# Performance work log

Hardware: AMD Instinct MI355X
Metric: run time of the kernel (lower is better)

Reference implementation:

```python
import jax, jax.numpy as jnp
import numpy as np

B, H, D, RD = 32, 16, 256, 64          # batch, heads, head_dim, rotary_dim
NE, NI = 4096, 16384                   # n_embd, n_inner
SLOTS, KVL = 32768, 1024               # paged cache slots, per-batch kv length
EPS = 1e-5


def setup_inputs() -> dict:
    key = jax.random.key(0)
    ks = jax.random.split(key, 12)
    s = 0.02
    return {
        "hidden_states": jax.random.normal(ks[0], (B, 1, NE), jnp.float32),
        "key_cache": jax.random.normal(ks[1], (SLOTS, H, D), jnp.float32),
        "value_cache": jax.random.normal(ks[2], (SLOTS, H, D), jnp.float32),
        "ln_w": jnp.ones((NE,), jnp.float32),
        "ln_b": jnp.zeros((NE,), jnp.float32),
        "wq": jax.random.normal(ks[3], (NE, NE), jnp.float32) * s,
        "wk": jax.random.normal(ks[4], (NE, NE), jnp.float32) * s,
        "wv": jax.random.normal(ks[5], (NE, NE), jnp.float32) * s,
        "wo": jax.random.normal(ks[6], (NE, NE), jnp.float32) * s,
        "fc_in_w": jax.random.normal(ks[7], (NE, NI), jnp.float32) * s,
        "fc_in_b": jnp.zeros((NI,), jnp.float32),
        "fc_out_w": jax.random.normal(ks[8], (NI, NE), jnp.float32) * s,
        "fc_out_b": jnp.zeros((NE,), jnp.float32),
        "attention_mask": jnp.zeros((B, 1, 1, KVL), jnp.float32),
        "new_key_location": jnp.arange(B, dtype=jnp.int32),
        "new_value_location": jnp.arange(B, dtype=jnp.int32),
        "past_valid_key_decode_indices": jax.random.randint(ks[9], (B, KVL), 0, SLOTS, jnp.int32),
        "past_valid_value_decode_indices": jax.random.randint(ks[10], (B, KVL), 0, SLOTS, jnp.int32),
        "position_ids": jax.random.randint(ks[11], (B, 1), 0, KVL, jnp.int32),
    }


def _rope(x, position_ids):
    # GPT-J rotate-every-two rotary on first RD dims. x: [B, S, H, D]
    half = RD // 2
    inv_freq = 1.0 / (10000.0 ** (jnp.arange(0, RD, 2, dtype=jnp.float32) / RD))  # [half]
    ang = position_ids.astype(jnp.float32)[..., None] * inv_freq  # [B, S, half]
    sin = jnp.sin(ang)[:, :, None, :]  # [B, S, 1, half]
    cos = jnp.cos(ang)[:, :, None, :]
    xr, xp = x[..., :RD], x[..., RD:]
    x1, x2 = xr[..., 0::2], xr[..., 1::2]
    o1 = x1 * cos - x2 * sin
    o2 = x2 * cos + x1 * sin
    rot = jnp.stack([o1, o2], axis=-1).reshape(xr.shape)
    return jnp.concatenate([rot, xp], axis=-1)


def reference(hidden_states, key_cache, value_cache, ln_w, ln_b, wq, wk, wv, wo,
              fc_in_w, fc_in_b, fc_out_w, fc_out_b, attention_mask,
              new_key_location, new_value_location,
              past_valid_key_decode_indices, past_valid_value_decode_indices,
              position_ids):
    residual = hidden_states[:, -1:, :]                       # [B, 1, NE]
    mu = jnp.mean(hidden_states, axis=-1, keepdims=True)
    var = jnp.mean(jnp.square(hidden_states - mu), axis=-1, keepdims=True)
    h = (hidden_states - mu) * jax.lax.rsqrt(var + EPS) * ln_w + ln_b

    q = (h @ wq).reshape(B, 1, H, D)
    k = (h @ wk).reshape(B, 1, H, D)
    v = (h @ wv).reshape(B, 1, H, D)
    q = _rope(q, position_ids)
    k = _rope(k, position_ids)

    # paged KV update: scatter new token, gather valid slots per batch
    kc = key_cache.at[new_key_location].set(k[:, 0])          # [SLOTS, H, D]
    vc = value_cache.at[new_value_location].set(v[:, 0])
    K = kc[past_valid_key_decode_indices]                     # [B, KVL, H, D]
    V = vc[past_valid_value_decode_indices]                   # [B, KVL, H, D]

    scale = jnp.asarray(np.sqrt(D), jnp.float32)
    scores = jnp.einsum("bqhd,blhd->bhql", q, K) / scale + attention_mask
    p = jax.nn.softmax(scores, axis=-1)                       # [B, H, 1, KVL]
    ctx = jnp.einsum("bhql,blhd->bqhd", p, V).reshape(B, 1, NE)
    attn_out = ctx @ wo

    m = jax.nn.gelu(h[:, -1:, :] @ fc_in_w + fc_in_b, approximate=True)
    mlp_out = m @ fc_out_w + fc_out_b

    return attn_out + mlp_out + residual
```

## Files before the change

### kernel.cpp

```cpp
#include <hip/hip_runtime.h>
#include <math.h>

#define BB 32
#define HH 16
#define DD 256
#define RDIM 64
#define NEMB 4096
#define NINT 16384
#define NSLOTS 32768
#define KVLEN 1024
#define LNEPS 1e-5f
#define NCH 16
#define CH 64

__global__ __launch_bounds__(256) void ln_kernel(const float* __restrict__ x,
    const float* __restrict__ lw, const float* __restrict__ lb,
    float* __restrict__ hT)
{
    int b = blockIdx.x;
    int t = threadIdx.x;
    const float* row = x + (size_t)b * NEMB;
    float4 v[4];
    float sum = 0.f, sq = 0.f;
#pragma unroll
    for (int j = 0; j < 4; ++j) {
        v[j] = *(const float4*)(row + t * 4 + j * 1024);
        sum += v[j].x + v[j].y + v[j].z + v[j].w;
        sq += v[j].x * v[j].x + v[j].y * v[j].y + v[j].z * v[j].z + v[j].w * v[j].w;
    }
    __shared__ float s1[4], s2[4];
#pragma unroll
    for (int o = 32; o > 0; o >>= 1) {
        sum += __shfl_xor(sum, o, 64);
        sq += __shfl_xor(sq, o, 64);
    }
    int wave = t >> 6, lane = t & 63;
    if (lane == 0) { s1[wave] = sum; s2[wave] = sq; }
    __syncthreads();
    sum = s1[0] + s1[1] + s1[2] + s1[3];
    sq = s2[0] + s2[1] + s2[2] + s2[3];
    float mu = sum / NEMB;
    float var = sq / NEMB - mu * mu;
    float rstd = rsqrtf(var + LNEPS);
#pragma unroll
    for (int j = 0; j < 4; ++j) {
        int n = t * 4 + j * 1024;
        float4 wv = *(const float4*)(lw + n);
        float4 bv = *(const float4*)(lb + n);
        hT[(size_t)(n + 0) * BB + b] = (v[j].x - mu) * rstd * wv.x + bv.x;
        hT[(size_t)(n + 1) * BB + b] = (v[j].y - mu) * rstd * wv.y + bv.y;
        hT[(size_t)(n + 2) * BB + b] = (v[j].z - mu) * rstd * wv.z + bv.z;
        hT[(size_t)(n + 3) * BB + b] = (v[j].w - mu) * rstd * wv.w + bv.w;
    }
}

__device__ __forceinline__ void gemm_body(const float* __restrict__ AT,
    const float* __restrict__ W, float* __restrict__ P,
    int N, int kChunk, int x, int s)
{
    int n = (x * 256 + threadIdx.x) * 2;
    size_t k0 = (size_t)s * kChunk;
    float2 acc[32];
#pragma unroll
    for (int mi = 0; mi < 32; ++mi) acc[mi] = make_float2(0.f, 0.f);
    const float* w = W + k0 * N + n;
    const float* a = AT + k0 * 32;
#pragma unroll 4
    for (int kk = 0; kk < kChunk; ++kk) {
        float2 wv = *(const float2*)w;
#pragma unroll
        for (int mi = 0; mi < 32; ++mi) {
            float am = a[mi];
            acc[mi].x = fmaf(am, wv.x, acc[mi].x);
            acc[mi].y = fmaf(am, wv.y, acc[mi].y);
        }
        w += N;
        a += 32;
    }
    float* p = P + ((size_t)s * 32) * N + n;
#pragma unroll
    for (int mi = 0; mi < 32; ++mi)
        *(float2*)(p + (size_t)mi * N) = acc[mi];
}

__global__ __launch_bounds__(256) void phase2_kernel(const float* __restrict__ hT,
    const float* __restrict__ wq, const float* __restrict__ wk, const float* __restrict__ wv,
    float* __restrict__ Pq, const float* __restrict__ fciw, float* __restrict__ P1)
{
    int id = blockIdx.x;
    if (id < 768) {
        int w = id >> 8;
        const float* W = (w == 0) ? wq : (w == 1) ? wk : wv;
        float* Pz = Pq + (size_t)w * ((size_t)32 * 32 * NEMB);
        gemm_body(hT, W, Pz, NEMB, 128, id & 7, (id >> 3) & 31);
    } else {
        id -= 768;
        gemm_body(hT, fciw, P1, NINT, 256, id & 31, id >> 5);
    }
}

__device__ inline float gelu_tanh(float x)
{
    float x3 = x * x * x;
    return 0.5f * x * (1.f + tanhf(0.7978845608028654f * (x + 0.044715f * x3)));
}

__global__ __launch_bounds__(256) void phase3_kernel(const float* __restrict__ Pq,
    float* __restrict__ q, float* __restrict__ k, float* __restrict__ v,
    const int* __restrict__ pos,
    const float* __restrict__ P1, const float* __restrict__ fcib, float* __restrict__ mT)
{
    int id = blockIdx.x, t = threadIdx.x;
    if (id < 768) {
        int w = id >> 8;
        int m = (id >> 3) & 31;
        int n0 = ((id & 7) * 256 + t) * 2;
        const float* p = Pq + (size_t)w * ((size_t)32 * 32 * NEMB) + (size_t)m * NEMB + n0;
        float sx = 0.f, sy = 0.f;
#pragma unroll 4
        for (int i = 0; i < 32; ++i) {
            float2 u = *(const float2*)p;
            sx += u.x; sy += u.y;
            p += (size_t)32 * NEMB;
        }
        int d = n0 & (DD - 1);
        if (w < 2 && d < RDIM) {
            int i = d >> 1;
            float fr = exp2f((float)i * (-13.287712379549449f / 32.f));
            float ang = (float)pos[m] * fr;
            float sn, cs;
            sincosf(ang, &sn, &cs);
            float x1 = sx, x2 = sy;
            sx = x1 * cs - x2 * sn;
            sy = x2 * cs + x1 * sn;
        }
        float* o = (w == 0) ? q : (w == 1) ? k : v;
        *(float2*)(o + (size_t)m * NEMB + n0) = make_float2(sx, sy);
    } else {
        int j = id - 768;
        int m = j >> 6;
        int n = (j & 63) * 256 + t;
        const float* p = P1 + (size_t)m * NINT + n;
        float s = 0.f;
#pragma unroll 4
        for (int i = 0; i < 16; ++i) { s += *p; p += (size_t)32 * NINT; }
        mT[(size_t)n * 32 + m] = gelu_tanh(s + fcib[n]);
    }
}

__global__ __launch_bounds__(256) void phase4_kernel(const float* __restrict__ q,
    const float* __restrict__ knew, const float* __restrict__ vnew,
    const float* __restrict__ kcache, const float* __restrict__ vcache,
    const int* __restrict__ kidx, const int* __restrict__ vidx,
    const int* __restrict__ nkl, const int* __restrict__ nvl,
    const float* __restrict__ mask,
    float* __restrict__ pm, float* __restrict__ pl, float* __restrict__ pctx,
    const float* __restrict__ mT, const float* __restrict__ fcow, float* __restrict__ P2)
{
    int id = blockIdx.x;
    if (id >= 8192) {
        int j = id - 8192;
        gemm_body(mT, fcow, P2, NEMB, 256, j & 7, j >> 3);
        return;
    }
    int bh = id >> 4, c = id & 15;
    int b = bh >> 4, h = bh & 15;
    int t = threadIdx.x;
    __shared__ float qs[DD];
    __shared__ float sc[CH];
    __shared__ const float* kp[CH];
    __shared__ const float* vp[CH];
    __shared__ float cx[4][DD];

    qs[t] = q[(size_t)b * NEMB + (size_t)h * DD + t];
    if (t < CH) {
        int l = c * CH + t;
        int ks = kidx[b * KVLEN + l];
        int vs = vidx[b * KVLEN + l];
        const float* kbase = kcache + (size_t)ks * NEMB;
        const float* vbase = vcache + (size_t)vs * NEMB;
#pragma unroll
        for (int j = 0; j < BB; ++j) {
            if (nkl[j] == ks) kbase = knew + (size_t)j * NEMB;
            if (nvl[j] == vs) vbase = vnew + (size_t)j * NEMB;
        }
        kp[t] = kbase + (size_t)h * DD;
        vp[t] = vbase + (size_t)h * DD;
    }
    __syncthreads();

    int wave = t >> 6, lane = t & 63;
    int g = lane >> 4, u = lane & 15;

    float4 qf[4];
#pragma unroll
    for (int j = 0; j < 4; ++j) qf[j] = *(const float4*)(qs + u * 4 + j * 64);

#pragma unroll
    for (int it = 0; it < 4; ++it) {
        int l = it * 16 + wave * 4 + g;
        const float* kr = kp[l];
        float d = 0.f;
#pragma unroll
        for (int j = 0; j < 4; ++j) {
            float4 kf = *(const float4*)(kr + u * 4 + j * 64);
            d = fmaf(kf.x, qf[j].x, fmaf(kf.y, qf[j].y, fmaf(kf.z, qf[j].z, fmaf(kf.w, qf[j].w, d))));
        }
        d += __shfl_xor(d, 8, 64);
        d += __shfl_xor(d, 4, 64);
        d += __shfl_xor(d, 2, 64);
        d += __shfl_xor(d, 1, 64);
        if (u == 0) sc[l] = d * 0.0625f + mask[b * KVLEN + c * CH + l];
    }
    __syncthreads();

    float sv = sc[lane];
    float mx = sv;
#pragma unroll
    for (int o = 32; o > 0; o >>= 1) mx = fmaxf(mx, __shfl_xor(mx, o, 64));
    float e = expf(sv - mx);
    float sm = e;
#pragma unroll
    for (int o = 32; o > 0; o >>= 1) sm += __shfl_xor(sm, o, 64);

    float4 a4 = make_float4(0.f, 0.f, 0.f, 0.f);
#pragma unroll 8
    for (int l = wave; l < CH; l += 4) {
        float4 vf = *(const float4*)(vp[l] + lane * 4);
        float pw = __shfl(e, l, 64);
        a4.x = fmaf(pw, vf.x, a4.x);
        a4.y = fmaf(pw, vf.y, a4.y);
        a4.z = fmaf(pw, vf.z, a4.z);
        a4.w = fmaf(pw, vf.w, a4.w);
    }
    *(float4*)(&cx[wave][lane * 4]) = a4;
    __syncthreads();

    int pi = bh * NCH + c;
    pctx[(size_t)pi * DD + t] = cx[0][t] + cx[1][t] + cx[2][t] + cx[3][t];
    if (t == 0) { pm[pi] = mx; pl[pi] = sm; }
}

__global__ __launch_bounds__(256) void attn_comb_kernel(const float* __restrict__ pm,
    const float* __restrict__ pl, const float* __restrict__ pctx,
    float* __restrict__ ctxT)
{
    int bh = blockIdx.x;
    int b = bh >> 4, h = bh & 15;
    int t = threadIdx.x;
    float M = -INFINITY;
#pragma unroll
    for (int c = 0; c < NCH; ++c) M = fmaxf(M, pm[bh * NCH + c]);
    float L = 0.f, acc = 0.f;
#pragma unroll
    for (int c = 0; c < NCH; ++c) {
        float wv = expf(pm[bh * NCH + c] - M);
        L += pl[bh * NCH + c] * wv;
        acc += pctx[((size_t)bh * NCH + c) * DD + t] * wv;
    }
    ctxT[((size_t)h * DD + t) * BB + b] = acc / L;
}

__global__ __launch_bounds__(256) void phase6_kernel(const float* __restrict__ ctxT,
    const float* __restrict__ wo, float* __restrict__ P0,
    const float* __restrict__ P2, const float* __restrict__ fcob,
    const float* __restrict__ resid, float* __restrict__ mlp_tmp)
{
    int id = blockIdx.x, t = threadIdx.x;
    if (id < 512) {
        gemm_body(ctxT, wo, P0, NEMB, 64, id & 7, id >> 3);
    } else {
        int j = id - 512;
        int m = j >> 4;
        int n = (j & 15) * 256 + t;
        const float* p = P2 + (size_t)m * NEMB + n;
        float s = 0.f;
#pragma unroll 4
        for (int i = 0; i < 64; ++i) { s += *p; p += (size_t)32 * NEMB; }
        mlp_tmp[(size_t)m * NEMB + n] = s + fcob[n] + resid[(size_t)m * NEMB + n];
    }
}

__global__ __launch_bounds__(256) void phase7_kernel(const float* __restrict__ P0,
    const float* __restrict__ mlp_tmp, float* __restrict__ out)
{
    int n = blockIdx.x * 256 + threadIdx.x;
    int m = blockIdx.y;
    const float* p = P0 + (size_t)m * NEMB + n;
    float s = 0.f;
#pragma unroll 4
    for (int i = 0; i < 64; ++i) { s += *p; p += (size_t)32 * NEMB; }
    out[(size_t)m * NEMB + n] = s + mlp_tmp[(size_t)m * NEMB + n];
}

extern "C" void kernel_launch(void* const* d_in, const int* in_sizes, int n_in,
                              void* d_out, int out_size, void* d_ws, size_t ws_size,
                              hipStream_t stream)
{
    (void)in_sizes; (void)n_in; (void)out_size; (void)ws_size;
    const float* hs      = (const float*)d_in[0];
    const float* kcache  = (const float*)d_in[1];
    const float* vcache  = (const float*)d_in[2];
    const float* ln_w    = (const float*)d_in[3];
    const float* ln_b    = (const float*)d_in[4];
    const float* wq      = (const float*)d_in[5];
    const float* wk      = (const float*)d_in[6];
    const float* wv      = (const float*)d_in[7];
    const float* wo      = (const float*)d_in[8];
    const float* fc_in_w = (const float*)d_in[9];
    const float* fc_in_b = (const float*)d_in[10];
    const float* fc_out_w= (const float*)d_in[11];
    const float* fc_out_b= (const float*)d_in[12];
    const float* mask    = (const float*)d_in[13];
    const int* nkl       = (const int*)d_in[14];
    const int* nvl       = (const int*)d_in[15];
    const int* kidx      = (const int*)d_in[16];
    const int* vidx      = (const int*)d_in[17];
    const int* pos       = (const int*)d_in[18];
    float* out = (float*)d_out;

    char* ws = (char*)d_ws;
    float* hT      = (float*)ws; ws += (size_t)NEMB * BB * 4;
    float* qb      = (float*)ws; ws += (size_t)BB * NEMB * 4;
    float* kb      = (float*)ws; ws += (size_t)BB * NEMB * 4;
    float* vb      = (float*)ws; ws += (size_t)BB * NEMB * 4;
    float* ctxT    = (float*)ws; ws += (size_t)NEMB * BB * 4;
    float* mlp_tmp = (float*)ws; ws += (size_t)BB * NEMB * 4;
    float* mT      = (float*)ws; ws += (size_t)NINT * BB * 4;
    float* pm      = (float*)ws; ws += (size_t)BB * HH * NCH * 4;
    float* pl      = (float*)ws; ws += (size_t)BB * HH * NCH * 4;
    float* pctx    = (float*)ws; ws += (size_t)BB * HH * NCH * DD * 4;
    float* Pq      = (float*)ws; ws += (size_t)3 * 32 * 32 * NEMB * 4;
    float* P0      = (float*)ws; ws += (size_t)64 * 32 * NEMB * 4;
    float* P1      = (float*)ws; ws += (size_t)16 * 32 * NINT * 4;
    float* P2      = (float*)ws;

    ln_kernel<<<BB, 256, 0, stream>>>(hs, ln_w, ln_b, hT);

    phase2_kernel<<<1280, 256, 0, stream>>>(hT, wq, wk, wv, Pq, fc_in_w, P1);

    phase3_kernel<<<2816, 256, 0, stream>>>(Pq, qb, kb, vb, pos, P1, fc_in_b, mT);

    phase4_kernel<<<8704, 256, 0, stream>>>(qb, kb, vb, kcache, vcache,
                                            kidx, vidx, nkl, nvl, mask,
                                            pm, pl, pctx, mT, fc_out_w, P2);

    attn_comb_kernel<<<BB * HH, 256, 0, stream>>>(pm, pl, pctx, ctxT);

    phase6_kernel<<<1024, 256, 0, stream>>>(ctxT, wo, P0, P2, fc_out_b, hs, mlp_tmp);

    phase7_kernel<<<dim3(16, 32), 256, 0, stream>>>(P0, mlp_tmp, out);
}
```

Measured before the change: 503.5 us.

## Shrink phase4 to single-wave blocks and reorder fc_out GEMM blocks first

Phase4 now runs with 64-thread blocks. Each attention chunk block is a single wave that does every score and value accumulation itself, which removes the shared q copy, the cross-wave context reduction and one barrier. The fc_out split-K GEMM is redistributed into 2048 64-thread blocks that are scheduled before the attention blocks, so the long GEMM work starts early. The risk is that each attention wave now does four times the serial work, and the smaller blocks may change occupancy and latency hiding.

```diff
diff --git a/kernel.cpp b/kernel.cpp
--- a/kernel.cpp
+++ b/kernel.cpp
@@ -83,6 +83,35 @@
         *(float2*)(p + (size_t)mi * N) = acc[mi];
 }
 
+__device__ __forceinline__ void gemm_body64(const float* __restrict__ AT,
+    const float* __restrict__ W, float* __restrict__ P,
+    int N, int kChunk, int x, int s)
+{
+    int n = (x * 64 + threadIdx.x) * 2;
+    size_t k0 = (size_t)s * kChunk;
+    float2 acc[32];
+#pragma unroll
+    for (int mi = 0; mi < 32; ++mi) acc[mi] = make_float2(0.f, 0.f);
+    const float* w = W + k0 * N + n;
+    const float* a = AT + k0 * 32;
+#pragma unroll 4
+    for (int kk = 0; kk < kChunk; ++kk) {
+        float2 wv = *(const float2*)w;
+#pragma unroll
+        for (int mi = 0; mi < 32; ++mi) {
+            float am = a[mi];
+            acc[mi].x = fmaf(am, wv.x, acc[mi].x);
+            acc[mi].y = fmaf(am, wv.y, acc[mi].y);
+        }
+        w += N;
+        a += 32;
+    }
+    float* p = P + ((size_t)s * 32) * N + n;
+#pragma unroll
+    for (int mi = 0; mi < 32; ++mi)
+        *(float2*)(p + (size_t)mi * N) = acc[mi];
+}
+
 __global__ __launch_bounds__(256) void phase2_kernel(const float* __restrict__ hT,
     const float* __restrict__ wq, const float* __restrict__ wk, const float* __restrict__ wv,
     float* __restrict__ Pq, const float* __restrict__ fciw, float* __restrict__ P1)
@@ -148,7 +177,7 @@
     }
 }
 
-__global__ __launch_bounds__(256) void phase4_kernel(const float* __restrict__ q,
+__global__ __launch_bounds__(64) void phase4_kernel(const float* __restrict__ q,
     const float* __restrict__ knew, const float* __restrict__ vnew,
     const float* __restrict__ kcache, const float* __restrict__ vcache,
     const int* __restrict__ kidx, const int* __restrict__ vidx,
@@ -158,25 +187,22 @@
     const float* __restrict__ mT, const float* __restrict__ fcow, float* __restrict__ P2)
 {
     int id = blockIdx.x;
-    if (id >= 8192) {
-        int j = id - 8192;
-        gemm_body(mT, fcow, P2, NEMB, 256, j & 7, j >> 3);
+    int t = threadIdx.x;
+    if (id < 2048) {
+        gemm_body64(mT, fcow, P2, NEMB, 256, id & 31, id >> 5);
         return;
     }
+    id -= 2048;
     int bh = id >> 4, c = id & 15;
     int b = bh >> 4, h = bh & 15;
-    int t = threadIdx.x;
-    __shared__ float qs[DD];
+
+    __shared__ const float* kparr[CH];
+    __shared__ const float* vparr[CH];
     __shared__ float sc[CH];
-    __shared__ const float* kp[CH];
-    __shared__ const float* vp[CH];
-    __shared__ float cx[4][DD];
-
-    qs[t] = q[(size_t)b * NEMB + (size_t)h * DD + t];
-    if (t < CH) {
-        int l = c * CH + t;
-        int ks = kidx[b * KVLEN + l];
-        int vs = vidx[b * KVLEN + l];
+
+    {
+        int ks = kidx[b * KVLEN + c * CH + t];
+        int vs = vidx[b * KVLEN + c * CH + t];
         const float* kbase = kcache + (size_t)ks * NEMB;
         const float* vbase = vcache + (size_t)vs * NEMB;
 #pragma unroll
@@ -184,22 +210,20 @@
             if (nkl[j] == ks) kbase = knew + (size_t)j * NEMB;
             if (nvl[j] == vs) vbase = vnew + (size_t)j * NEMB;
         }
-        kp[t] = kbase + (size_t)h * DD;
-        vp[t] = vbase + (size_t)h * DD;
+        kparr[t] = kbase + (size_t)h * DD;
+        vparr[t] = vbase + (size_t)h * DD;
     }
     __syncthreads();
 
-    int wave = t >> 6, lane = t & 63;
-    int g = lane >> 4, u = lane & 15;
-
+    int u = t & 15, g = t >> 4;
     float4 qf[4];
 #pragma unroll
-    for (int j = 0; j < 4; ++j) qf[j] = *(const float4*)(qs + u * 4 + j * 64);
-
-#pragma unroll
-    for (int it = 0; it < 4; ++it) {
-        int l = it * 16 + wave * 4 + g;
-        const float* kr = kp[l];
+    for (int j = 0; j < 4; ++j) qf[j] = *(const float4*)(q + (size_t)b * NEMB + (size_t)h * DD + u * 4 + j * 64);
+
+#pragma unroll 4
+    for (int it = 0; it < 16; ++it) {
+        int l = it * 4 + g;
+        const float* kr = kparr[l];
         float d = 0.f;
 #pragma unroll
         for (int j = 0; j < 4; ++j) {
@@ -214,7 +238,7 @@
     }
     __syncthreads();
 
-    float sv = sc[lane];
+    float sv = sc[t];
     float mx = sv;
 #pragma unroll
     for (int o = 32; o > 0; o >>= 1) mx = fmaxf(mx, __shfl_xor(mx, o, 64));
@@ -225,19 +249,18 @@
 
     float4 a4 = make_float4(0.f, 0.f, 0.f, 0.f);
 #pragma unroll 8
-    for (int l = wave; l < CH; l += 4) {
-        float4 vf = *(const float4*)(vp[l] + lane * 4);
+    for (int l = 0; l < CH; ++l) {
+        const float* vr = vparr[l];
+        float4 vf = *(const float4*)(vr + t * 4);
         float pw = __shfl(e, l, 64);
         a4.x = fmaf(pw, vf.x, a4.x);
         a4.y = fmaf(pw, vf.y, a4.y);
         a4.z = fmaf(pw, vf.z, a4.z);
         a4.w = fmaf(pw, vf.w, a4.w);
     }
-    *(float4*)(&cx[wave][lane * 4]) = a4;
-    __syncthreads();
 
     int pi = bh * NCH + c;
-    pctx[(size_t)pi * DD + t] = cx[0][t] + cx[1][t] + cx[2][t] + cx[3][t];
+    *(float4*)(pctx + (size_t)pi * DD + t * 4) = a4;
     if (t == 0) { pm[pi] = mx; pl[pi] = sm; }
 }
 
@@ -341,7 +364,7 @@
 
     phase3_kernel<<<2816, 256, 0, stream>>>(Pq, qb, kb, vb, pos, P1, fc_in_b, mT);
 
-    phase4_kernel<<<8704, 256, 0, stream>>>(qb, kb, vb, kcache, vcache,
+    phase4_kernel<<<10240, 64, 0, stream>>>(qb, kb, vb, kcache, vcache,
                                             kidx, vidx, nkl, nvl, mask,
                                             pm, pl, pctx, mT, fc_out_w, P2);
 
```

Result: faster. 448.0 us (-11.0%).

## Process all heads per attention block over contiguous KV rows

Applied to the files above, without the earlier changes.

The attention kernel is regridded so each block handles one batch element and a 32-position KV chunk across all 16 heads, instead of one (batch, head) pair over 64 positions. Each 16-thread group owns one head. Slot-index lookup, new-token redirection and mask loads are done once per position rather than once per head, and each gathered KV row is read as a full contiguous 16 KB slot. The fc_out GEMM blocks are moved to the start of the grid. Splitting into 32 chunks doubles the partial softmax state that the combine kernel must merge. The score and probability exchanges rely on wave-level lockstep and have no explicit barrier.

```diff
diff --git a/kernel.cpp b/kernel.cpp
--- a/kernel.cpp
+++ b/kernel.cpp
@@ -10,8 +10,8 @@
 #define NSLOTS 32768
 #define KVLEN 1024
 #define LNEPS 1e-5f
-#define NCH 16
-#define CH 64
+#define NCH 32
+#define CHR 32
 
 __global__ __launch_bounds__(256) void ln_kernel(const float* __restrict__ x,
     const float* __restrict__ lw, const float* __restrict__ lb,
@@ -158,23 +158,22 @@
     const float* __restrict__ mT, const float* __restrict__ fcow, float* __restrict__ P2)
 {
     int id = blockIdx.x;
-    if (id >= 8192) {
-        int j = id - 8192;
-        gemm_body(mT, fcow, P2, NEMB, 256, j & 7, j >> 3);
+    int t = threadIdx.x;
+    if (id < 512) {
+        gemm_body(mT, fcow, P2, NEMB, 256, id & 7, id >> 3);
         return;
     }
-    int bh = id >> 4, c = id & 15;
-    int b = bh >> 4, h = bh & 15;
-    int t = threadIdx.x;
-    __shared__ float qs[DD];
-    __shared__ float sc[CH];
-    __shared__ const float* kp[CH];
-    __shared__ const float* vp[CH];
-    __shared__ float cx[4][DD];
-
-    qs[t] = q[(size_t)b * NEMB + (size_t)h * DD + t];
-    if (t < CH) {
-        int l = c * CH + t;
+    id -= 512;
+    int b = id >> 5, c = id & 31;
+
+    __shared__ const float* kp[CHR];
+    __shared__ const float* vp[CHR];
+    __shared__ float msk[CHR];
+    __shared__ float sc[CHR * HH];
+    __shared__ float pe[CHR * HH];
+
+    if (t < CHR) {
+        int l = c * CHR + t;
         int ks = kidx[b * KVLEN + l];
         int vs = vidx[b * KVLEN + l];
         const float* kbase = kcache + (size_t)ks * NEMB;
@@ -184,61 +183,85 @@
             if (nkl[j] == ks) kbase = knew + (size_t)j * NEMB;
             if (nvl[j] == vs) vbase = vnew + (size_t)j * NEMB;
         }
-        kp[t] = kbase + (size_t)h * DD;
-        vp[t] = vbase + (size_t)h * DD;
+        kp[t] = kbase;
+        vp[t] = vbase;
+        msk[t] = mask[b * KVLEN + l];
     }
     __syncthreads();
 
-    int wave = t >> 6, lane = t & 63;
-    int g = lane >> 4, u = lane & 15;
+    int h = t >> 4, u = t & 15;
+    int off = h * DD + u * 16;
 
     float4 qf[4];
-#pragma unroll
-    for (int j = 0; j < 4; ++j) qf[j] = *(const float4*)(qs + u * 4 + j * 64);
-
-#pragma unroll
-    for (int it = 0; it < 4; ++it) {
-        int l = it * 16 + wave * 4 + g;
-        const float* kr = kp[l];
-        float d = 0.f;
+    const float* qrow = q + (size_t)b * NEMB + off;
+#pragma unroll
+    for (int j = 0; j < 4; ++j) qf[j] = *(const float4*)(qrow + j * 4);
+
+#pragma unroll 2
+    for (int l = 0; l < CHR; l += 2) {
+        const float* k0 = kp[l] + off;
+        const float* k1 = kp[l + 1] + off;
+        float4 ka[4], kb4[4];
+#pragma unroll
+        for (int j = 0; j < 4; ++j) ka[j] = *(const float4*)(k0 + j * 4);
+#pragma unroll
+        for (int j = 0; j < 4; ++j) kb4[j] = *(const float4*)(k1 + j * 4);
+        float d0 = 0.f, d1 = 0.f;
 #pragma unroll
         for (int j = 0; j < 4; ++j) {
-            float4 kf = *(const float4*)(kr + u * 4 + j * 64);
-            d = fmaf(kf.x, qf[j].x, fmaf(kf.y, qf[j].y, fmaf(kf.z, qf[j].z, fmaf(kf.w, qf[j].w, d))));
-        }
-        d += __shfl_xor(d, 8, 64);
-        d += __shfl_xor(d, 4, 64);
-        d += __shfl_xor(d, 2, 64);
-        d += __shfl_xor(d, 1, 64);
-        if (u == 0) sc[l] = d * 0.0625f + mask[b * KVLEN + c * CH + l];
-    }
-    __syncthreads();
-
-    float sv = sc[lane];
-    float mx = sv;
-#pragma unroll
-    for (int o = 32; o > 0; o >>= 1) mx = fmaxf(mx, __shfl_xor(mx, o, 64));
-    float e = expf(sv - mx);
-    float sm = e;
-#pragma unroll
-    for (int o = 32; o > 0; o >>= 1) sm += __shfl_xor(sm, o, 64);
-
-    float4 a4 = make_float4(0.f, 0.f, 0.f, 0.f);
-#pragma unroll 8
-    for (int l = wave; l < CH; l += 4) {
-        float4 vf = *(const float4*)(vp[l] + lane * 4);
-        float pw = __shfl(e, l, 64);
-        a4.x = fmaf(pw, vf.x, a4.x);
-        a4.y = fmaf(pw, vf.y, a4.y);
-        a4.z = fmaf(pw, vf.z, a4.z);
-        a4.w = fmaf(pw, vf.w, a4.w);
-    }
-    *(float4*)(&cx[wave][lane * 4]) = a4;
-    __syncthreads();
-
-    int pi = bh * NCH + c;
-    pctx[(size_t)pi * DD + t] = cx[0][t] + cx[1][t] + cx[2][t] + cx[3][t];
-    if (t == 0) { pm[pi] = mx; pl[pi] = sm; }
+            d0 = fmaf(ka[j].x, qf[j].x, fmaf(ka[j].y, qf[j].y, fmaf(ka[j].z, qf[j].z, fmaf(ka[j].w, qf[j].w, d0))));
+            d1 = fmaf(kb4[j].x, qf[j].x, fmaf(kb4[j].y, qf[j].y, fmaf(kb4[j].z, qf[j].z, fmaf(kb4[j].w, qf[j].w, d1))));
+        }
+#pragma unroll
+        for (int o = 8; o > 0; o >>= 1) {
+            d0 += __shfl_xor(d0, o, 64);
+            d1 += __shfl_xor(d1, o, 64);
+        }
+        if (u == 0) {
+            sc[l * HH + h] = d0 * 0.0625f + msk[l];
+            sc[(l + 1) * HH + h] = d1 * 0.0625f + msk[l + 1];
+        }
+    }
+
+    float v0 = sc[(2 * u) * HH + h];
+    float v1 = sc[(2 * u + 1) * HH + h];
+    float mx = fmaxf(v0, v1);
+#pragma unroll
+    for (int o = 8; o > 0; o >>= 1) mx = fmaxf(mx, __shfl_xor(mx, o, 64));
+    float e0 = expf(v0 - mx), e1 = expf(v1 - mx);
+    float sm = e0 + e1;
+#pragma unroll
+    for (int o = 8; o > 0; o >>= 1) sm += __shfl_xor(sm, o, 64);
+    pe[(2 * u) * HH + h] = e0;
+    pe[(2 * u + 1) * HH + h] = e1;
+
+    float4 acc[4];
+#pragma unroll
+    for (int j = 0; j < 4; ++j) acc[j] = make_float4(0.f, 0.f, 0.f, 0.f);
+    for (int l = 0; l < CHR; l += 2) {
+        const float* r0 = vp[l] + off;
+        const float* r1 = vp[l + 1] + off;
+        float4 va[4], vb4[4];
+#pragma unroll
+        for (int j = 0; j < 4; ++j) va[j] = *(const float4*)(r0 + j * 4);
+#pragma unroll
+        for (int j = 0; j < 4; ++j) vb4[j] = *(const float4*)(r1 + j * 4);
+        float pw0 = pe[l * HH + h];
+        float pw1 = pe[(l + 1) * HH + h];
+#pragma unroll
+        for (int j = 0; j < 4; ++j) {
+            acc[j].x = fmaf(pw0, va[j].x, fmaf(pw1, vb4[j].x, acc[j].x));
+            acc[j].y = fmaf(pw0, va[j].y, fmaf(pw1, vb4[j].y, acc[j].y));
+            acc[j].z = fmaf(pw0, va[j].z, fmaf(pw1, vb4[j].z, acc[j].z));
+            acc[j].w = fmaf(pw0, va[j].w, fmaf(pw1, vb4[j].w, acc[j].w));
+        }
+    }
+
+    int pi = (b * HH + h) * NCH + c;
+    float* po = pctx + (size_t)pi * DD + u * 16;
+#pragma unroll
+    for (int j = 0; j < 4; ++j) *(float4*)(po + j * 4) = acc[j];
+    if (u == 0) { pm[pi] = mx; pl[pi] = sm; }
 }
 
 __global__ __launch_bounds__(256) void attn_comb_kernel(const float* __restrict__ pm,
@@ -341,7 +364,7 @@
 
     phase3_kernel<<<2816, 256, 0, stream>>>(Pq, qb, kb, vb, pos, P1, fc_in_b, mT);
 
-    phase4_kernel<<<8704, 256, 0, stream>>>(qb, kb, vb, kcache, vcache,
+    phase4_kernel<<<1536, 256, 0, stream>>>(qb, kb, vb, kcache, vcache,
                                             kidx, vidx, nkl, nvl, mask,
                                             pm, pl, pctx, mT, fc_out_w, P2);
 
```

Measured after the change: 541.9 us. 1.08x slower.
